# Kernel tuning notes

Measured on AMD Instinct MI355X. Metric: run time of the kernel, lower is better.

Reference implementation:

```python
import jax, jax.numpy as jnp
import numpy as np

B, IN, HS, NM = 256, 512, 512, 1

def setup_inputs() -> dict:
    key = jax.random.key(0)
    ks = jax.random.split(key, 12)
    def kaiming(k, shape):
        fan_in = shape[0]
        bound = float(np.sqrt(6.0 / fan_in))  # kaiming_uniform with a=sqrt(5) approx; use gain sqrt(2): bound = sqrt(6/fan_in)
        return jax.random.uniform(k, shape, jnp.float32, -bound, bound)
    return {
        "x_t":  jax.random.normal(ks[0], (B, IN), jnp.float32),
        "h_t":  jax.random.normal(ks[1], (B, HS), jnp.float32),
        "c_t":  jax.random.normal(ks[2], (B, HS), jnp.float32),
        "hebb": jax.random.normal(ks[3], (B, HS, HS), jnp.float32) * 0.1,
        "W":    kaiming(ks[4], (IN, 4 * HS)),
        "U":    kaiming(ks[5], (HS, 4 * HS)),
        "bias": jnp.zeros((4 * HS,), jnp.float32),
        "alpha": jax.random.normal(ks[6], (1, 1, HS), jnp.float32) * 1e-4,
        "nm_w": jax.random.normal(ks[7], (NM, HS), jnp.float32),
        "nm_b": jnp.zeros((NM,), jnp.float32),
        "mt_w": jax.random.normal(ks[8], (HS, NM), jnp.float32),
        "mt_b": jnp.zeros((HS,), jnp.float32),
    }

def reference(x_t, h_t, c_t, hebb, W, U, bias, alpha, nm_w, nm_b, mt_w, mt_b):
    # g_t_hebb = h_t (B,1,HS) @ (alpha*hebb) (B,HS,HS) -> (B,HS)
    g_t_hebb = jnp.einsum('bh,bhk->bk', h_t, alpha * hebb)
    gates = x_t @ W + h_t @ U + bias                        # (B, 4*HS)
    i_t = jax.nn.sigmoid(gates[:, :HS])
    f_t = jax.nn.sigmoid(gates[:, HS:2 * HS])
    g_t = jnp.tanh(gates[:, 2 * HS:3 * HS] + g_t_hebb)
    o_t = jax.nn.sigmoid(gates[:, 3 * HS:])
    # rank-1 outer product per batch element: (B,HS,1)@(B,1,HS)
    delta_hebb = jnp.einsum('bi,bj->bij', h_t, g_t)         # (B,HS,HS)
    m_t = jnp.tanh(h_t @ nm_w.T + nm_b)                     # (B,NM)
    m_t = m_t @ mt_w.T + mt_b                               # (B,HS)
    hebb_new = jnp.clip(hebb + m_t[:, None, :] * delta_hebb, -2.0, 2.0)
    c_new = f_t * c_t + i_t * g_t
    h_new = o_t * jnp.tanh(c_new)
    return h_new, c_new, hebb_new
```

## Files before the change

kernel.cpp:

```cpp
#include <hip/hip_runtime.h>
#include <math.h>


__device__ __forceinline__ float sigm(float x) { return 1.0f / (1.0f + __expf(-x)); }
__device__ __forceinline__ float clip2(float v) { return fminf(fmaxf(v, -2.0f), 2.0f); }

__global__ __launch_bounds__(256, 4)
void gates_gemm(const float* __restrict__ x, const float* __restrict__ h,
                const float* __restrict__ W, const float* __restrict__ U,
                const float* __restrict__ bias, float* __restrict__ gates)
{
    __shared__ float As[64][64];
    __shared__ float Bs[64][40];

    const int t     = threadIdx.x;
    const int bcol0 = blockIdx.x * 32;
    const int brow0 = blockIdx.y * 64;
    const int row   = t & 63;
    const int cg    = t >> 6;

    float acc[8] = {};

    for (int ks = 0; ks < 16; ++ks) {
        const float* srcA;
        const float* srcB;
        int ka;
        if (ks < 8) { srcA = x; srcB = W; ka = ks * 64; }
        else        { srcA = h; srcB = U; ka = ks * 64 - 512; }

        float4 av[4];
        #pragma unroll
        for (int m = 0; m < 4; ++m)
            av[m] = *(const float4*)&srcA[(size_t)(brow0 + row) * 512 + ka + cg * 16 + m * 4];
        const int kr0 = t >> 3;
        const int c4  = t & 7;
        float4 bv0 = *(const float4*)&srcB[(size_t)(ka + kr0)      * 2048 + bcol0 + c4 * 4];
        float4 bv1 = *(const float4*)&srcB[(size_t)(ka + kr0 + 32) * 2048 + bcol0 + c4 * 4];

        __syncthreads();
        #pragma unroll
        for (int m = 0; m < 4; ++m) {
            As[cg * 16 + m * 4 + 0][row] = av[m].x;
            As[cg * 16 + m * 4 + 1][row] = av[m].y;
            As[cg * 16 + m * 4 + 2][row] = av[m].z;
            As[cg * 16 + m * 4 + 3][row] = av[m].w;
        }
        *(float4*)&Bs[kr0][c4 * 4]      = bv0;
        *(float4*)&Bs[kr0 + 32][c4 * 4] = bv1;
        __syncthreads();

        #pragma unroll
        for (int k = 0; k < 64; ++k) {
            const float a = As[k][row];
            const float4 b0 = *(const float4*)&Bs[k][cg * 8];
            const float4 b1 = *(const float4*)&Bs[k][cg * 8 + 4];
            acc[0] += a * b0.x; acc[1] += a * b0.y; acc[2] += a * b0.z; acc[3] += a * b0.w;
            acc[4] += a * b1.x; acc[5] += a * b1.y; acc[6] += a * b1.z; acc[7] += a * b1.w;
        }
    }

    const int colb = bcol0 + cg * 8;
    float4 o0, o1;
    o0.x = acc[0] + bias[colb + 0]; o0.y = acc[1] + bias[colb + 1];
    o0.z = acc[2] + bias[colb + 2]; o0.w = acc[3] + bias[colb + 3];
    o1.x = acc[4] + bias[colb + 4]; o1.y = acc[5] + bias[colb + 5];
    o1.z = acc[6] + bias[colb + 6]; o1.w = acc[7] + bias[colb + 7];
    float* gp = &gates[(size_t)(brow0 + row) * 2048 + colb];
    *(float4*)gp       = o0;
    *(float4*)(gp + 4) = o1;
}

__global__ __launch_bounds__(512, 4)
void hebb_fused(const float* __restrict__ h_t, const float* __restrict__ c_t,
                const float* __restrict__ hebb, const float* __restrict__ alpha,
                const float* __restrict__ nm_w, const float* __restrict__ nm_b,
                const float* __restrict__ mt_w, const float* __restrict__ mt_b,
                const float* __restrict__ gates, float* __restrict__ out)
{
    const int b   = blockIdx.x >> 3;
    const int jt  = blockIdx.x & 7;
    const int j0  = jt * 64;
    const int t   = threadIdx.x;
    const int tj4 = t & 15;
    const int ti  = t >> 4;

    __shared__ float hsh[512];
    __shared__ float red[32][64];
    __shared__ float upd[64];
    __shared__ float redm[512];
    __shared__ float msh;

    const float4* hb    = (const float4*)(hebb + (size_t)b * 262144);
    const int     cbase = jt * 16 + tj4;
    float4 r[16];
    #pragma unroll
    for (int k = 0; k < 16; ++k)
        r[k] = hb[(size_t)(ti * 16 + k) * 128 + cbase];

    const float hv0 = h_t[(size_t)b * 512 + t];
    hsh[t]  = hv0;
    redm[t] = hv0 * nm_w[t];
    __syncthreads();

    if (t < 64) {
        float v = 0.f;
        #pragma unroll
        for (int q = 0; q < 8; ++q) v += redm[t + q * 64];
        #pragma unroll
        for (int off = 32; off > 0; off >>= 1) v += __shfl_down(v, off);
        if (t == 0) msh = tanhf(v + nm_b[0]);
    }

    float4 ps = {0.f, 0.f, 0.f, 0.f};
    #pragma unroll
    for (int k = 0; k < 16; ++k) {
        const float hv = hsh[ti * 16 + k];
        ps.x += hv * r[k].x;
        ps.y += hv * r[k].y;
        ps.z += hv * r[k].z;
        ps.w += hv * r[k].w;
    }
    *(float4*)&red[ti][tj4 * 4] = ps;
    __syncthreads();

    if (t < 64) {
        float s = 0.f;
        #pragma unroll
        for (int q = 0; q < 32; ++q) s += red[q][t];
        const int j = j0 + t;
        const size_t gbase = (size_t)b * 2048;
        const float g  = tanhf(gates[gbase + 1024 + j] + alpha[j] * s);
        const float mm = msh * mt_w[j] + mt_b[j];
        upd[t] = mm * g;
        const float it_ = sigm(gates[gbase + j]);
        const float ft  = sigm(gates[gbase + 512 + j]);
        const float ot  = sigm(gates[gbase + 1536 + j]);
        const float cn  = ft * c_t[(size_t)b * 512 + j] + it_ * g;
        out[(size_t)b * 512 + j]          = ot * tanhf(cn);
        out[131072 + (size_t)b * 512 + j] = cn;
    }
    __syncthreads();

    const float4 u = *(const float4*)&upd[tj4 * 4];
    float4* ho = (float4*)(out + 262144 + (size_t)b * 262144);
    #pragma unroll
    for (int k = 0; k < 16; ++k) {
        const float hv = hsh[ti * 16 + k];
        float4 w;
        w.x = clip2(r[k].x + u.x * hv);
        w.y = clip2(r[k].y + u.y * hv);
        w.z = clip2(r[k].z + u.z * hv);
        w.w = clip2(r[k].w + u.w * hv);
        ho[(size_t)(ti * 16 + k) * 128 + cbase] = w;
    }
}

extern "C" void kernel_launch(void* const* d_in, const int* in_sizes, int n_in,
                              void* d_out, int out_size, void* d_ws, size_t ws_size,
                              hipStream_t stream)
{
    const float* x_t   = (const float*)d_in[0];
    const float* h_t   = (const float*)d_in[1];
    const float* c_t   = (const float*)d_in[2];
    const float* hebb  = (const float*)d_in[3];
    const float* W     = (const float*)d_in[4];
    const float* U     = (const float*)d_in[5];
    const float* bias  = (const float*)d_in[6];
    const float* alpha = (const float*)d_in[7];
    const float* nm_w  = (const float*)d_in[8];
    const float* nm_b  = (const float*)d_in[9];
    const float* mt_w  = (const float*)d_in[10];
    const float* mt_b  = (const float*)d_in[11];
    float* out   = (float*)d_out;
    float* gates = (float*)d_ws;

    dim3 g1(64, 4);
    gates_gemm<<<g1, 256, 0, stream>>>(x_t, h_t, W, U, bias, gates);
    hebb_fused<<<2048, 512, 0, stream>>>(h_t, c_t, hebb, alpha, nm_w, nm_b,
                                         mt_w, mt_b, gates, out);
}
```

Baseline: 507.8 us.

## Split hebb kernel into 32-column tiles with fewer registers and more blocks

The hebb_fused kernel now handles 32 columns per block instead of 64, doubling the grid to 4096 blocks. Each thread holds 8 float4 of hebb instead of 16, which cuts register pressure, and the launch bound asks for 8 waves per SIMD. The column reduction is split across two half-warps and combined with a shuffle. tanhf is replaced by an exp-based fast tanh. The aim is higher occupancy, so more memory requests are in flight for this bandwidth-bound streaming of hebb. The cost is that the per-block nm reduction and the gate loads are repeated across twice as many blocks.

```diff
diff --git a/kernel.cpp b/kernel.cpp
--- a/kernel.cpp
+++ b/kernel.cpp
@@ -3,6 +3,7 @@
 
 
 __device__ __forceinline__ float sigm(float x) { return 1.0f / (1.0f + __expf(-x)); }
+__device__ __forceinline__ float tanh_fast(float x) { return 1.0f - 2.0f / (1.0f + __expf(2.0f * x)); }
 __device__ __forceinline__ float clip2(float v) { return fminf(fmaxf(v, -2.0f), 2.0f); }
 
 __global__ __launch_bounds__(256, 4)
@@ -70,36 +71,37 @@
     *(float4*)(gp + 4) = o1;
 }
 
-__global__ __launch_bounds__(512, 4)
+__global__ __launch_bounds__(512, 8)
 void hebb_fused(const float* __restrict__ h_t, const float* __restrict__ c_t,
                 const float* __restrict__ hebb, const float* __restrict__ alpha,
                 const float* __restrict__ nm_w, const float* __restrict__ nm_b,
                 const float* __restrict__ mt_w, const float* __restrict__ mt_b,
                 const float* __restrict__ gates, float* __restrict__ out)
 {
-    const int b   = blockIdx.x >> 3;
-    const int jt  = blockIdx.x & 7;
-    const int j0  = jt * 64;
+    const int b   = blockIdx.x >> 4;
+    const int jt  = blockIdx.x & 15;
     const int t   = threadIdx.x;
-    const int tj4 = t & 15;
-    const int ti  = t >> 4;
+    const int tj4 = t & 7;
+    const int ti  = t >> 3;
 
-    __shared__ float hsh[512];
-    __shared__ float red[32][64];
-    __shared__ float upd[64];
+    __shared__ __align__(16) float hsh[512];
     __shared__ float redm[512];
+    __shared__ __align__(16) float red[64][36];
+    __shared__ __align__(16) float upd[32];
     __shared__ float msh;
 
+    const float hv0 = h_t[(size_t)b * 512 + t];
+    const float nw  = nm_w[t];
+
     const float4* hb    = (const float4*)(hebb + (size_t)b * 262144);
-    const int     cbase = jt * 16 + tj4;
-    float4 r[16];
+    const int     cbase = jt * 8 + tj4;
+    float4 r[8];
     #pragma unroll
-    for (int k = 0; k < 16; ++k)
-        r[k] = hb[(size_t)(ti * 16 + k) * 128 + cbase];
+    for (int k = 0; k < 8; ++k)
+        r[k] = hb[(size_t)(ti * 8 + k) * 128 + cbase];
 
-    const float hv0 = h_t[(size_t)b * 512 + t];
     hsh[t]  = hv0;
-    redm[t] = hv0 * nm_w[t];
+    redm[t] = hv0 * nw;
     __syncthreads();
 
     if (t < 64) {
@@ -108,13 +110,13 @@
         for (int q = 0; q < 8; ++q) v += redm[t + q * 64];
         #pragma unroll
         for (int off = 32; off > 0; off >>= 1) v += __shfl_down(v, off);
-        if (t == 0) msh = tanhf(v + nm_b[0]);
+        if (t == 0) msh = tanh_fast(v + nm_b[0]);
     }
 
     float4 ps = {0.f, 0.f, 0.f, 0.f};
     #pragma unroll
-    for (int k = 0; k < 16; ++k) {
-        const float hv = hsh[ti * 16 + k];
+    for (int k = 0; k < 8; ++k) {
+        const float hv = hsh[ti * 8 + k];
         ps.x += hv * r[k].x;
         ps.y += hv * r[k].y;
         ps.z += hv * r[k].z;
@@ -124,34 +126,39 @@
     __syncthreads();
 
     if (t < 64) {
+        const int c  = t & 31;
+        const int hf = t >> 5;
         float s = 0.f;
         #pragma unroll
-        for (int q = 0; q < 32; ++q) s += red[q][t];
-        const int j = j0 + t;
-        const size_t gbase = (size_t)b * 2048;
-        const float g  = tanhf(gates[gbase + 1024 + j] + alpha[j] * s);
-        const float mm = msh * mt_w[j] + mt_b[j];
-        upd[t] = mm * g;
-        const float it_ = sigm(gates[gbase + j]);
-        const float ft  = sigm(gates[gbase + 512 + j]);
-        const float ot  = sigm(gates[gbase + 1536 + j]);
-        const float cn  = ft * c_t[(size_t)b * 512 + j] + it_ * g;
-        out[(size_t)b * 512 + j]          = ot * tanhf(cn);
-        out[131072 + (size_t)b * 512 + j] = cn;
+        for (int q = 0; q < 32; ++q) s += red[hf * 32 + q][c];
+        s += __shfl_xor(s, 32);
+        if (hf == 0) {
+            const int j = jt * 32 + c;
+            const size_t gb = (size_t)b * 2048;
+            const float g  = tanh_fast(gates[gb + 1024 + j] + alpha[j] * s);
+            const float mm = msh * mt_w[j] + mt_b[j];
+            upd[c] = mm * g;
+            const float it_ = sigm(gates[gb + j]);
+            const float ft  = sigm(gates[gb + 512 + j]);
+            const float ot  = sigm(gates[gb + 1536 + j]);
+            const float cn  = ft * c_t[(size_t)b * 512 + j] + it_ * g;
+            out[(size_t)b * 512 + j]          = ot * tanh_fast(cn);
+            out[131072 + (size_t)b * 512 + j] = cn;
+        }
     }
     __syncthreads();
 
     const float4 u = *(const float4*)&upd[tj4 * 4];
     float4* ho = (float4*)(out + 262144 + (size_t)b * 262144);
     #pragma unroll
-    for (int k = 0; k < 16; ++k) {
-        const float hv = hsh[ti * 16 + k];
+    for (int k = 0; k < 8; ++k) {
+        const float hv = hsh[ti * 8 + k];
         float4 w;
         w.x = clip2(r[k].x + u.x * hv);
         w.y = clip2(r[k].y + u.y * hv);
         w.z = clip2(r[k].z + u.z * hv);
         w.w = clip2(r[k].w + u.w * hv);
-        ho[(size_t)(ti * 16 + k) * 128 + cbase] = w;
+        ho[(size_t)(ti * 8 + k) * 128 + cbase] = w;
     }
 }
 
@@ -176,6 +183,6 @@
 
     dim3 g1(64, 4);
     gates_gemm<<<g1, 256, 0, stream>>>(x_t, h_t, W, U, bias, gates);
-    hebb_fused<<<2048, 512, 0, stream>>>(h_t, c_t, hebb, alpha, nm_w, nm_b,
+    hebb_fused<<<4096, 512, 0, stream>>>(h_t, c_t, hebb, alpha, nm_w, nm_b,
                                          mt_w, mt_b, gates, out);
 }
```

New measurement: 512.1 us. No clear change (+0.9%).
